# Kernel tuning notes

Hardware: AMD Instinct MI355X
Metric: run time of the kernel (lower is better)

Reference implementation:

```python
import jax, jax.numpy as jnp
import numpy as np

DIM = 1024
HEADS = 16
HEAD_DIM = DIM // HEADS
HIDDEN = 4 * DIM
EPS = 1e-6


def _layer_norm(x, scale, bias):
    mu = jnp.mean(x, axis=-1, keepdims=True)
    var = jnp.mean(jnp.square(x - mu), axis=-1, keepdims=True)
    return (x - mu) * jax.lax.rsqrt(var + EPS) * scale + bias


def setup_inputs() -> dict:
    key = jax.random.key(0)
    ks = jax.random.split(key, 8)
    s = 0.02
    return {
        "x": jax.random.normal(ks[0], (8, 1024, DIM), dtype=jnp.float32),
        "w_qkv": jax.random.normal(ks[1], (DIM, 3 * DIM), dtype=jnp.float32) * s,
        "b_qkv": jnp.zeros((3 * DIM,), jnp.float32),
        "w_proj": jax.random.normal(ks[2], (DIM, DIM), dtype=jnp.float32) * s,
        "b_proj": jnp.zeros((DIM,), jnp.float32),
        "ln1_scale": jnp.ones((DIM,), jnp.float32),
        "ln1_bias": jnp.zeros((DIM,), jnp.float32),
        "ln2_scale": jnp.ones((DIM,), jnp.float32),
        "ln2_bias": jnp.zeros((DIM,), jnp.float32),
        "w_fc1": jax.random.normal(ks[3], (DIM, HIDDEN), dtype=jnp.float32) * s,
        "b_fc1": jnp.zeros((HIDDEN,), jnp.float32),
        "w_fc2": jax.random.normal(ks[4], (HIDDEN, DIM), dtype=jnp.float32) * s,
        "b_fc2": jnp.zeros((DIM,), jnp.float32),
    }


def reference(x, w_qkv, b_qkv, w_proj, b_proj, ln1_scale, ln1_bias,
              ln2_scale, ln2_bias, w_fc1, b_fc1, w_fc2, b_fc2):
    B, N, C = x.shape
    scale = HEAD_DIM ** -0.5

    # --- attention branch ---
    h = _layer_norm(x, ln1_scale, ln1_bias)
    qkv = h @ w_qkv + b_qkv                          # [B,N,3C]
    qkv = qkv.reshape(B, N, 3, HEADS, HEAD_DIM)
    qkv = jnp.transpose(qkv, (2, 0, 3, 1, 4))        # [3,B,H,N,D]
    q, k, v = qkv[0], qkv[1], qkv[2]
    attn = jnp.einsum("bhnd,bhmd->bhnm", q, k) * scale
    attn = jax.nn.softmax(attn, axis=-1)
    o = jnp.einsum("bhnm,bhmd->bhnd", attn, v)       # [B,H,N,D]
    o = jnp.transpose(o, (0, 2, 1, 3)).reshape(B, N, C)
    x = x + (o @ w_proj + b_proj)

    # --- mlp branch ---
    h = _layer_norm(x, ln2_scale, ln2_bias)
    h = jax.nn.gelu(h @ w_fc1 + b_fc1)               # tanh approx, matches flax default
    x = x + (h @ w_fc2 + b_fc2)
    return x
```

## Files before the change

kernel.cpp:

```cpp
#include <hip/hip_runtime.h>

typedef __attribute__((ext_vector_type(8))) short short8;
typedef __attribute__((ext_vector_type(4))) float f32x4;
typedef unsigned short ushort;
typedef unsigned int uint;

#define DIM 1024
#define NSEQ 1024
#define BATCH 8
#define HEADS 16
#define HD 64
#define HIDDEN 4096
#define NROWS (BATCH * NSEQ)

__device__ inline ushort f2bf(float f) {
  uint u = __float_as_uint(f);
  u += 0x7fff + ((u >> 16) & 1);
  return (ushort)(u >> 16);
}

__device__ inline f32x4 zero4() {
  f32x4 z; z[0] = 0.f; z[1] = 0.f; z[2] = 0.f; z[3] = 0.f; return z;
}

__device__ inline float gelu_fast(float x) {
  float u2 = 1.5957691216057308f * (x + 0.044715f * x * x * x);
  float e = __builtin_amdgcn_exp2f(-1.4426950408889634f * u2);
  return x / (1.0f + e);
}

#define GLDS16(g, l)                                                  \
  __builtin_amdgcn_global_load_lds(                                   \
      (const __attribute__((address_space(1))) void*)(g),             \
      (__attribute__((address_space(3))) void*)(l), 16, 0, 0)

__global__ __launch_bounds__(256) void ln_kernel(
    const float* __restrict__ x, const float* __restrict__ sc,
    const float* __restrict__ bi, ushort* __restrict__ out) {
  int row = blockIdx.x;
  int t = threadIdx.x;
  const float4 v = reinterpret_cast<const float4*>(x + (size_t)row * DIM)[t];
  float s = v.x + v.y + v.z + v.w;
  float s2 = v.x * v.x + v.y * v.y + v.z * v.z + v.w * v.w;
#pragma unroll
  for (int off = 32; off >= 1; off >>= 1) {
    s += __shfl_xor(s, off);
    s2 += __shfl_xor(s2, off);
  }
  __shared__ float ps[4], ps2[4];
  int w = t >> 6;
  if ((t & 63) == 0) { ps[w] = s; ps2[w] = s2; }
  __syncthreads();
  s = ps[0] + ps[1] + ps[2] + ps[3];
  s2 = ps2[0] + ps2[1] + ps2[2] + ps2[3];
  float mu = s * (1.0f / DIM);
  float var = s2 * (1.0f / DIM) - mu * mu;
  float rstd = rsqrtf(var + 1e-6f);
  float4 scv = reinterpret_cast<const float4*>(sc)[t];
  float4 biv = reinterpret_cast<const float4*>(bi)[t];
  ushort4 o;
  o.x = f2bf((v.x - mu) * rstd * scv.x + biv.x);
  o.y = f2bf((v.y - mu) * rstd * scv.y + biv.y);
  o.z = f2bf((v.z - mu) * rstd * scv.z + biv.z);
  o.w = f2bf((v.w - mu) * rstd * scv.w + biv.w);
  reinterpret_cast<ushort4*>(out + (size_t)row * DIM)[t] = o;
}

__global__ __launch_bounds__(256) void wtrans_kernel(
    const float* __restrict__ w, ushort* __restrict__ wt, int K, int N) {
  __shared__ float tile[32][33];
  int n0 = blockIdx.x * 32, k0 = blockIdx.y * 32;
  int tx = threadIdx.x & 31, ty = threadIdx.x >> 5;
#pragma unroll
  for (int j = 0; j < 4; j++)
    tile[ty + 8 * j][tx] = w[(size_t)(k0 + ty + 8 * j) * N + n0 + tx];
  __syncthreads();
#pragma unroll
  for (int j = 0; j < 4; j++)
    wt[(size_t)(n0 + ty + 8 * j) * K + k0 + tx] = f2bf(tile[tx][ty + 8 * j]);
}

__global__ __launch_bounds__(256) void vtrans_kernel(
    const ushort* __restrict__ qkv, ushort* __restrict__ vT) {
  __shared__ ushort Ts[64 * 64];
  int bh = blockIdx.y;
  int b = bh >> 4, h = bh & 15;
  int n0 = blockIdx.x * 64;
  int t = threadIdx.x;
  const ushort* src = qkv + (size_t)b * NSEQ * 3072 + 2048 + h * 64;
#pragma unroll
  for (int i = 0; i < 2; i++) {
    int ci = i * 256 + t;
    int rr = ci >> 3, c = ci & 7;
    short8 v = *reinterpret_cast<const short8*>(src + (size_t)(n0 + rr) * 3072 + c * 8);
    *reinterpret_cast<short8*>(&Ts[rr * 64 + ((c ^ (rr >> 3)) & 7) * 8]) = v;
  }
  __syncthreads();
  ushort* dst = vT + (size_t)bh * 64 * NSEQ;
#pragma unroll
  for (int i = 0; i < 2; i++) {
    int ci = i * 256 + t;
    int dd = ci >> 3, c = ci & 7;
    short8 v;
#pragma unroll
    for (int j = 0; j < 8; j++) {
      int nn = c * 8 + j;
      v[j] = (short)Ts[nn * 64 + (((dd >> 3) ^ (nn >> 3)) & 7) * 8 + (dd & 7)];
    }
    *reinterpret_cast<short8*>(dst + (size_t)dd * NSEQ + n0 + c * 8) = v;
  }
}

template <int BN, int EPI>
__global__ __launch_bounds__(512, 2) void gemm256_kernel(
    const ushort* __restrict__ A, const ushort* __restrict__ Bt,
    const float* __restrict__ bias, const float* __restrict__ res,
    void* __restrict__ outp, int M, int N, int K) {
  constexpr int BM = 256, BK = 32;
  constexpr int WM = (BN == 256) ? 2 : 4;
  constexpr int WN = 8 / WM;
  constexpr int MR = (BM / WM) / 16;
  constexpr int NR = (BN / WN) / 16;
  constexpr int AR = 2;
  constexpr int BR = BN / 128;

  __shared__ ushort As[2][BM * BK];
  __shared__ ushort Bs[2][BN * BK];

  int t = threadIdx.x, lane = t & 63, w = t >> 6;
  int wr = w / WN, wc = w % WN;
  int r = lane & 15, g = lane >> 4;
  int m0 = blockIdx.y * BM, n0 = blockIdx.x * BN;
  const ushort* Ab = A + (size_t)m0 * K;
  const ushort* Bb = Bt + (size_t)n0 * K;

  int srow = t >> 2;
  int sgc8 = ((t & 3) ^ (srow & 3)) * 8;
  int swb = (w << 4) * BK;

  f32x4 acc[MR][NR];
#pragma unroll
  for (int mi = 0; mi < MR; mi++)
#pragma unroll
    for (int ni = 0; ni < NR; ni++) acc[mi][ni] = zero4();

  int nkt = K / BK;
#pragma unroll
  for (int p = 0; p < AR; p++)
    GLDS16(Ab + (size_t)(p * 128 + srow) * K + sgc8, &As[0][p * 128 * BK + swb]);
#pragma unroll
  for (int p = 0; p < BR; p++)
    GLDS16(Bb + (size_t)(p * 128 + srow) * K + sgc8, &Bs[0][p * 128 * BK + swb]);
  __syncthreads();

  int cur = 0;
  for (int kt = 0; kt < nkt; kt++) {
    if (kt + 1 < nkt) {
      int ko = (kt + 1) * BK;
#pragma unroll
      for (int p = 0; p < AR; p++)
        GLDS16(Ab + (size_t)(p * 128 + srow) * K + ko + sgc8,
               &As[cur ^ 1][p * 128 * BK + swb]);
#pragma unroll
      for (int p = 0; p < BR; p++)
        GLDS16(Bb + (size_t)(p * 128 + srow) * K + ko + sgc8,
               &Bs[cur ^ 1][p * 128 * BK + swb]);
    }
    short8 a[MR], b[NR];
    int sw = (g ^ (r & 3)) * 8;
#pragma unroll
    for (int mi = 0; mi < MR; mi++)
      a[mi] = *reinterpret_cast<const short8*>(
          &As[cur][(wr * (BM / WM) + mi * 16 + r) * BK + sw]);
#pragma unroll
    for (int ni = 0; ni < NR; ni++)
      b[ni] = *reinterpret_cast<const short8*>(
          &Bs[cur][(wc * (BN / WN) + ni * 16 + r) * BK + sw]);
#pragma unroll
    for (int mi = 0; mi < MR; mi++)
#pragma unroll
      for (int ni = 0; ni < NR; ni++)
        acc[mi][ni] = __builtin_amdgcn_mfma_f32_16x16x32_bf16(a[mi], b[ni], acc[mi][ni], 0, 0, 0);
    __syncthreads();
    cur ^= 1;
  }

  int rg = g * 4;
#pragma unroll
  for (int mi = 0; mi < MR; mi++) {
#pragma unroll
    for (int ni = 0; ni < NR; ni++) {
      int row = m0 + wr * (BM / WM) + mi * 16 + rg;
      int col = n0 + wc * (BN / WN) + ni * 16 + r;
      float bv = bias[col];
#pragma unroll
      for (int j = 0; j < 4; j++) {
        float v = acc[mi][ni][j] + bv;
        if (EPI == 1) v = gelu_fast(v);
        if (EPI == 2) {
          reinterpret_cast<float*>(outp)[(size_t)(row + j) * N + col] =
              v + res[(size_t)(row + j) * N + col];
        } else {
          reinterpret_cast<ushort*>(outp)[(size_t)(row + j) * N + col] = f2bf(v);
        }
      }
    }
  }
}

#define SM_SCALE_L2E 0.18033688f
#define SM_BIAS_L2E 11.54156036f
__global__ __launch_bounds__(256) void attn_kernel(
    const ushort* __restrict__ qkv, const ushort* __restrict__ vT,
    ushort* __restrict__ o) {
  __shared__ ushort Kt[64 * 72];
  __shared__ ushort Vt[64 * 72];
  __shared__ ushort Pl[4][16 * 72];
  int q0 = blockIdx.x * 64, h = blockIdx.y, b = blockIdx.z;
  int t = threadIdx.x, lane = t & 63, w = t >> 6;
  int r = lane & 15, g = lane >> 4;
  const ushort* base = qkv + (size_t)b * NSEQ * 3072 + h * 64;
  const ushort* vbase = vT + (size_t)(b * HEADS + h) * 64 * NSEQ;

  short8 qf[2];
  {
    const ushort* qrow = base + (size_t)(q0 + w * 16 + r) * 3072;
    qf[0] = *reinterpret_cast<const short8*>(qrow + g * 8);
    qf[1] = *reinterpret_cast<const short8*>(qrow + 32 + g * 8);
  }

  float l[4] = {0.f, 0.f, 0.f, 0.f};
  f32x4 oacc[4];
#pragma unroll
  for (int db = 0; db < 4; db++) oacc[db] = zero4();

  int srw = t >> 3, sc8 = (t & 7) * 8;
  for (int kt = 0; kt < NSEQ / 64; kt++) {
    int k0 = kt * 64;
    short8 kreg[2], vreg[2];
#pragma unroll
    for (int i = 0; i < 2; i++) {
      int rw = srw + i * 32;
      kreg[i] = *reinterpret_cast<const short8*>(base + 1024 + (size_t)(k0 + rw) * 3072 + sc8);
      vreg[i] = *reinterpret_cast<const short8*>(vbase + (size_t)rw * NSEQ + k0 + sc8);
    }
    __syncthreads();
#pragma unroll
    for (int i = 0; i < 2; i++) {
      int rw = srw + i * 32;
      *reinterpret_cast<short8*>(&Kt[rw * 72 + sc8]) = kreg[i];
      *reinterpret_cast<short8*>(&Vt[rw * 72 + sc8]) = vreg[i];
    }
    __syncthreads();

#pragma unroll
    for (int kb = 0; kb < 4; kb++) {
      short8 kf0 = *reinterpret_cast<const short8*>(&Kt[(kb * 16 + r) * 72 + g * 8]);
      short8 kf1 = *reinterpret_cast<const short8*>(&Kt[(kb * 16 + r) * 72 + 32 + g * 8]);
      f32x4 z = zero4();
      z = __builtin_amdgcn_mfma_f32_16x16x32_bf16(qf[0], kf0, z, 0, 0, 0);
      z = __builtin_amdgcn_mfma_f32_16x16x32_bf16(qf[1], kf1, z, 0, 0, 0);
#pragma unroll
      for (int j = 0; j < 4; j++) {
        float p = __builtin_amdgcn_exp2f(fmaf(z[j], SM_SCALE_L2E, -SM_BIAS_L2E));
        l[j] += p;
        Pl[w][(g * 4 + j) * 72 + kb * 16 + r] = (ushort)(__float_as_uint(p) >> 16);
      }
    }

#pragma unroll
    for (int ks = 0; ks < 2; ks++) {
      short8 pa = *reinterpret_cast<const short8*>(&Pl[w][r * 72 + ks * 32 + g * 8]);
#pragma unroll
      for (int db = 0; db < 4; db++) {
        short8 vb = *reinterpret_cast<const short8*>(&Vt[(db * 16 + r) * 72 + ks * 32 + g * 8]);
        oacc[db] = __builtin_amdgcn_mfma_f32_16x16x32_bf16(pa, vb, oacc[db], 0, 0, 0);
      }
    }
  }

#pragma unroll
  for (int j = 0; j < 4; j++) {
#pragma unroll
    for (int off = 8; off >= 1; off >>= 1) l[j] += __shfl_xor(l[j], off);
    l[j] = 1.0f / l[j];
  }

#pragma unroll
  for (int db = 0; db < 4; db++)
#pragma unroll
    for (int j = 0; j < 4; j++) {
      size_t row = (size_t)b * NSEQ + q0 + w * 16 + g * 4 + j;
      int col = h * 64 + db * 16 + r;
      o[row * DIM + col] = f2bf(oacc[db][j] * l[j]);
    }
}

extern "C" void kernel_launch(void* const* d_in, const int* in_sizes, int n_in,
                              void* d_out, int out_size, void* d_ws, size_t ws_size,
                              hipStream_t stream) {
  const float* x      = (const float*)d_in[0];
  const float* w_qkv  = (const float*)d_in[1];
  const float* b_qkv  = (const float*)d_in[2];
  const float* w_proj = (const float*)d_in[3];
  const float* b_proj = (const float*)d_in[4];
  const float* ln1s   = (const float*)d_in[5];
  const float* ln1b   = (const float*)d_in[6];
  const float* ln2s   = (const float*)d_in[7];
  const float* ln2b   = (const float*)d_in[8];
  const float* w_fc1  = (const float*)d_in[9];
  const float* b_fc1  = (const float*)d_in[10];
  const float* w_fc2  = (const float*)d_in[11];
  const float* b_fc2  = (const float*)d_in[12];
  float* out = (float*)d_out;

  char* ws = (char*)d_ws;
  ushort* wqkv_t  = (ushort*)(ws);
  ushort* wproj_t = (ushort*)(ws + 6291456);
  ushort* wfc1_t  = (ushort*)(ws + 8388608);
  ushort* wfc2_t  = (ushort*)(ws + 16777216);
  ushort* hbuf    = (ushort*)(ws + 25165824);
  float*  x1      = (float*)(ws + 41943040);
  ushort* vTb     = (ushort*)(ws + 41943040);
  ushort* qkv     = (ushort*)(ws + 75497472);
  ushort* obuf    = (ushort*)(ws + 125829120);
  ushort* fc1a    = qkv;

  wtrans_kernel<<<dim3(3072 / 32, 1024 / 32), 256, 0, stream>>>(w_qkv, wqkv_t, 1024, 3072);
  wtrans_kernel<<<dim3(1024 / 32, 1024 / 32), 256, 0, stream>>>(w_proj, wproj_t, 1024, 1024);
  wtrans_kernel<<<dim3(4096 / 32, 1024 / 32), 256, 0, stream>>>(w_fc1, wfc1_t, 1024, 4096);
  wtrans_kernel<<<dim3(1024 / 32, 4096 / 32), 256, 0, stream>>>(w_fc2, wfc2_t, 4096, 1024);

  ln_kernel<<<NROWS, 256, 0, stream>>>(x, ln1s, ln1b, hbuf);
  gemm256_kernel<128, 0><<<dim3(3072 / 128, NROWS / 256), 512, 0, stream>>>(
      hbuf, wqkv_t, b_qkv, nullptr, qkv, NROWS, 3072, 1024);
  vtrans_kernel<<<dim3(NSEQ / 64, BATCH * HEADS), 256, 0, stream>>>(qkv, vTb);
  attn_kernel<<<dim3(NSEQ / 64, HEADS, BATCH), 256, 0, stream>>>(qkv, vTb, obuf);
  gemm256_kernel<128, 2><<<dim3(1024 / 128, NROWS / 256), 512, 0, stream>>>(
      obuf, wproj_t, b_proj, x, x1, NROWS, 1024, 1024);

  ln_kernel<<<NROWS, 256, 0, stream>>>(x1, ln2s, ln2b, hbuf);
  gemm256_kernel<256, 1><<<dim3(4096 / 256, NROWS / 256), 512, 0, stream>>>(
      hbuf, wfc1_t, b_fc1, nullptr, fc1a, NROWS, 4096, 1024);
  gemm256_kernel<128, 2><<<dim3(1024 / 128, NROWS / 256), 512, 0, stream>>>(
      fc1a, wfc2_t, b_fc2, x1, out, NROWS, 1024, 4096);
}
```

Baseline: 460.6 us.

## Deepen GEMM pipeline to four LDS stages with phased MFMA and tile swizzle

Replaces the double-buffered GEMM main loop with a 4-slot LDS ring that keeps three k-tiles in flight, using explicit vmcnt waits and split phases that interleave global-to-LDS loads with MFMA bursts under raised wave priority. It also remaps workgroup IDs so consecutive blocks share operand tiles in cache, and changes the LDS XOR swizzle to cut bank conflicts. The aim is to hide global load latency and improve L2 reuse. The cost is doubled LDS use, which may lower occupancy, and the hand-counted waitcnt values are fragile.

```diff
diff --git a/kernel.cpp b/kernel.cpp
--- a/kernel.cpp
+++ b/kernel.cpp
@@ -33,6 +33,8 @@
   __builtin_amdgcn_global_load_lds(                                   \
       (const __attribute__((address_space(1))) void*)(g),             \
       (__attribute__((address_space(3))) void*)(l), 16, 0, 0)
+
+#define WAITVM(n) asm volatile("s_waitcnt vmcnt(" #n ")" ::: "memory")
 
 __global__ __launch_bounds__(256) void ln_kernel(
     const float* __restrict__ x, const float* __restrict__ sc,
@@ -121,22 +123,48 @@
   constexpr int WN = 8 / WM;
   constexpr int MR = (BM / WM) / 16;
   constexpr int NR = (BN / WN) / 16;
+  constexpr int PH = MR / 4;
   constexpr int AR = 2;
   constexpr int BR = BN / 128;
-
-  __shared__ ushort As[2][BM * BK];
-  __shared__ ushort Bs[2][BN * BK];
+  static_assert(BN == 256 || BN == 128, "");
+
+  __shared__ ushort As[4][BM * BK];
+  __shared__ ushort Bs[4][BN * BK];
 
   int t = threadIdx.x, lane = t & 63, w = t >> 6;
   int wr = w / WN, wc = w % WN;
   int r = lane & 15, g = lane >> 4;
-  int m0 = blockIdx.y * BM, n0 = blockIdx.x * BN;
+
+  int nwg = gridDim.x * gridDim.y;
+  int flat = blockIdx.y * gridDim.x + blockIdx.x;
+  int swzf = (flat & 7) * (nwg >> 3) + (flat >> 3);
+  int bx = swzf % gridDim.x, by = swzf / gridDim.x;
+  int m0 = by * BM, n0 = bx * BN;
+
   const ushort* Ab = A + (size_t)m0 * K;
   const ushort* Bb = Bt + (size_t)n0 * K;
 
   int srow = t >> 2;
-  int sgc8 = ((t & 3) ^ (srow & 3)) * 8;
+  int sgc8 = (((t & 3) ^ (srow & 3) ^ ((srow >> 2) & 3)) & 3) * 8;
   int swb = (w << 4) * BK;
+  int sw = ((g ^ (r & 3) ^ ((r >> 2) & 3)) & 3) * 8;
+
+  auto stageA = [&](int kt2) {
+    ushort* as = &As[kt2 & 3][0];
+    int ko = kt2 * BK;
+#pragma unroll
+    for (int p = 0; p < AR; p++)
+      GLDS16(Ab + (size_t)(p * 128 + srow) * K + ko + sgc8,
+             as + p * 128 * BK + swb);
+  };
+  auto stageB = [&](int kt2) {
+    ushort* bs = &Bs[kt2 & 3][0];
+    int ko = kt2 * BK;
+#pragma unroll
+    for (int p = 0; p < BR; p++)
+      GLDS16(Bb + (size_t)(p * 128 + srow) * K + ko + sgc8,
+             bs + p * 128 * BK + swb);
+  };
 
   f32x4 acc[MR][NR];
 #pragma unroll
@@ -145,44 +173,61 @@
     for (int ni = 0; ni < NR; ni++) acc[mi][ni] = zero4();
 
   int nkt = K / BK;
-#pragma unroll
-  for (int p = 0; p < AR; p++)
-    GLDS16(Ab + (size_t)(p * 128 + srow) * K + sgc8, &As[0][p * 128 * BK + swb]);
-#pragma unroll
-  for (int p = 0; p < BR; p++)
-    GLDS16(Bb + (size_t)(p * 128 + srow) * K + sgc8, &Bs[0][p * 128 * BK + swb]);
-  __syncthreads();
-
-  int cur = 0;
+
+  stageA(0); stageB(0);
+  stageA(1); stageB(1);
+  stageA(2); stageB(2);
+  if constexpr (BN == 256) WAITVM(8); else WAITVM(6);
+  __builtin_amdgcn_s_barrier();
+  asm volatile("" ::: "memory");
+
   for (int kt = 0; kt < nkt; kt++) {
-    if (kt + 1 < nkt) {
-      int ko = (kt + 1) * BK;
-#pragma unroll
-      for (int p = 0; p < AR; p++)
-        GLDS16(Ab + (size_t)(p * 128 + srow) * K + ko + sgc8,
-               &As[cur ^ 1][p * 128 * BK + swb]);
-#pragma unroll
-      for (int p = 0; p < BR; p++)
-        GLDS16(Bb + (size_t)(p * 128 + srow) * K + ko + sgc8,
-               &Bs[cur ^ 1][p * 128 * BK + swb]);
-    }
-    short8 a[MR], b[NR];
-    int sw = (g ^ (r & 3)) * 8;
-#pragma unroll
-    for (int mi = 0; mi < MR; mi++)
-      a[mi] = *reinterpret_cast<const short8*>(
-          &As[cur][(wr * (BM / WM) + mi * 16 + r) * BK + sw]);
-#pragma unroll
-    for (int ni = 0; ni < NR; ni++)
-      b[ni] = *reinterpret_cast<const short8*>(
-          &Bs[cur][(wc * (BN / WN) + ni * 16 + r) * BK + sw]);
-#pragma unroll
-    for (int mi = 0; mi < MR; mi++)
-#pragma unroll
-      for (int ni = 0; ni < NR; ni++)
-        acc[mi][ni] = __builtin_amdgcn_mfma_f32_16x16x32_bf16(a[mi], b[ni], acc[mi][ni], 0, 0, 0);
-    __syncthreads();
-    cur ^= 1;
+    const ushort* as = &As[kt & 3][0];
+    const ushort* bs = &Bs[kt & 3][0];
+    short8 b[NR];
+#pragma unroll
+    for (int ph = 0; ph < PH; ph++) {
+      if (ph == 0) {
+#pragma unroll
+        for (int ni = 0; ni < NR; ni++)
+          b[ni] = *reinterpret_cast<const short8*>(
+              &bs[(wc * (BN / WN) + ni * 16 + r) * BK + sw]);
+      }
+      short8 a[4];
+#pragma unroll
+      for (int i = 0; i < 4; i++)
+        a[i] = *reinterpret_cast<const short8*>(
+            &as[(wr * (BM / WM) + (ph * 4 + i) * 16 + r) * BK + sw]);
+      if (kt + 3 < nkt) {
+        if constexpr (PH == 2) {
+          if (ph == 0) stageA(kt + 3); else stageB(kt + 3);
+        } else {
+          stageA(kt + 3); stageB(kt + 3);
+        }
+      }
+      if (ph == PH - 1) {
+        if (kt + 3 < nkt) {
+          if constexpr (BN == 256) WAITVM(8); else WAITVM(6);
+        } else if (kt + 2 < nkt) {
+          if constexpr (BN == 256) WAITVM(4); else WAITVM(3);
+        } else if (kt + 1 < nkt) {
+          WAITVM(0);
+        }
+      }
+      __builtin_amdgcn_s_barrier();
+      asm volatile("s_waitcnt lgkmcnt(0)" ::: "memory");
+      __builtin_amdgcn_sched_barrier(0);
+      __builtin_amdgcn_s_setprio(1);
+#pragma unroll
+      for (int i = 0; i < 4; i++)
+#pragma unroll
+        for (int ni = 0; ni < NR; ni++)
+          acc[ph * 4 + i][ni] = __builtin_amdgcn_mfma_f32_16x16x32_bf16(
+              a[i], b[ni], acc[ph * 4 + i][ni], 0, 0, 0);
+      __builtin_amdgcn_s_setprio(0);
+      __builtin_amdgcn_s_barrier();
+      asm volatile("" ::: "memory");
+    }
   }
 
   int rg = g * 4;
```

After: 398.8 us. -13.4%, faster.

## Switch GEMMs to 128x128 tiles with workgroup swizzle and stronger LDS swizzle

Applied to the files above, without the earlier changes.

Replaces the 256-row GEMM tiles (512 threads) with a 128x128 tile kernel of 256 threads and four waves. Each wave computes a 64x64 sub-tile. Block indices are remapped with an XCD-style swizzle so neighbouring blocks land on the same L2, and the LDS XOR pattern now also mixes in row bits to cut bank conflicts. Smaller tiles give more blocks and better occupancy, at the cost of lower arithmetic intensity and more global/L2 traffic per FLOP.

```diff
diff --git a/kernel.cpp b/kernel.cpp
--- a/kernel.cpp
+++ b/kernel.cpp
@@ -111,46 +111,46 @@
   }
 }
 
-template <int BN, int EPI>
-__global__ __launch_bounds__(512, 2) void gemm256_kernel(
+template <int EPI>
+__global__ __launch_bounds__(256, 3) void gemm128_kernel(
     const ushort* __restrict__ A, const ushort* __restrict__ Bt,
     const float* __restrict__ bias, const float* __restrict__ res,
     void* __restrict__ outp, int M, int N, int K) {
-  constexpr int BM = 256, BK = 32;
-  constexpr int WM = (BN == 256) ? 2 : 4;
-  constexpr int WN = 8 / WM;
-  constexpr int MR = (BM / WM) / 16;
-  constexpr int NR = (BN / WN) / 16;
-  constexpr int AR = 2;
-  constexpr int BR = BN / 128;
+  constexpr int BM = 128, BN = 128, BK = 32;
 
   __shared__ ushort As[2][BM * BK];
   __shared__ ushort Bs[2][BN * BK];
 
   int t = threadIdx.x, lane = t & 63, w = t >> 6;
-  int wr = w / WN, wc = w % WN;
+  int wr = w >> 1, wc = w & 1;
   int r = lane & 15, g = lane >> 4;
-  int m0 = blockIdx.y * BM, n0 = blockIdx.x * BN;
+
+  int nwg = gridDim.x * gridDim.y;
+  int flat = blockIdx.y * gridDim.x + blockIdx.x;
+  int swzf = (flat & 7) * (nwg >> 3) + (flat >> 3);
+  int bx = swzf % gridDim.x, by = swzf / gridDim.x;
+  int m0 = by * BM, n0 = bx * BN;
+
   const ushort* Ab = A + (size_t)m0 * K;
   const ushort* Bb = Bt + (size_t)n0 * K;
 
   int srow = t >> 2;
-  int sgc8 = ((t & 3) ^ (srow & 3)) * 8;
-  int swb = (w << 4) * BK;
-
-  f32x4 acc[MR][NR];
-#pragma unroll
-  for (int mi = 0; mi < MR; mi++)
-#pragma unroll
-    for (int ni = 0; ni < NR; ni++) acc[mi][ni] = zero4();
+  int sgc8 = (((t & 3) ^ (srow & 3) ^ ((srow >> 2) & 3)) & 3) * 8;
+  int swb = (t >> 6) * 16 * BK;
+  int sw = ((g ^ (r & 3) ^ ((r >> 2) & 3)) & 3) * 8;
+
+  f32x4 acc[4][4];
+#pragma unroll
+  for (int mi = 0; mi < 4; mi++)
+#pragma unroll
+    for (int ni = 0; ni < 4; ni++) acc[mi][ni] = zero4();
 
   int nkt = K / BK;
 #pragma unroll
-  for (int p = 0; p < AR; p++)
-    GLDS16(Ab + (size_t)(p * 128 + srow) * K + sgc8, &As[0][p * 128 * BK + swb]);
-#pragma unroll
-  for (int p = 0; p < BR; p++)
-    GLDS16(Bb + (size_t)(p * 128 + srow) * K + sgc8, &Bs[0][p * 128 * BK + swb]);
+  for (int p = 0; p < 2; p++) {
+    GLDS16(Ab + (size_t)(p * 64 + srow) * K + sgc8, &As[0][(p * 64) * BK + swb]);
+    GLDS16(Bb + (size_t)(p * 64 + srow) * K + sgc8, &Bs[0][(p * 64) * BK + swb]);
+  }
   __syncthreads();
 
   int cur = 0;
@@ -158,40 +158,39 @@
     if (kt + 1 < nkt) {
       int ko = (kt + 1) * BK;
 #pragma unroll
-      for (int p = 0; p < AR; p++)
-        GLDS16(Ab + (size_t)(p * 128 + srow) * K + ko + sgc8,
-               &As[cur ^ 1][p * 128 * BK + swb]);
-#pragma unroll
-      for (int p = 0; p < BR; p++)
-        GLDS16(Bb + (size_t)(p * 128 + srow) * K + ko + sgc8,
-               &Bs[cur ^ 1][p * 128 * BK + swb]);
-    }
-    short8 a[MR], b[NR];
-    int sw = (g ^ (r & 3)) * 8;
-#pragma unroll
-    for (int mi = 0; mi < MR; mi++)
+      for (int p = 0; p < 2; p++) {
+        GLDS16(Ab + (size_t)(p * 64 + srow) * K + ko + sgc8,
+               &As[cur ^ 1][(p * 64) * BK + swb]);
+        GLDS16(Bb + (size_t)(p * 64 + srow) * K + ko + sgc8,
+               &Bs[cur ^ 1][(p * 64) * BK + swb]);
+      }
+    }
+    short8 a[4], b[4];
+#pragma unroll
+    for (int mi = 0; mi < 4; mi++)
       a[mi] = *reinterpret_cast<const short8*>(
-          &As[cur][(wr * (BM / WM) + mi * 16 + r) * BK + sw]);
-#pragma unroll
-    for (int ni = 0; ni < NR; ni++)
+          &As[cur][(wr * 64 + mi * 16 + r) * BK + sw]);
+#pragma unroll
+    for (int ni = 0; ni < 4; ni++)
       b[ni] = *reinterpret_cast<const short8*>(
-          &Bs[cur][(wc * (BN / WN) + ni * 16 + r) * BK + sw]);
-#pragma unroll
-    for (int mi = 0; mi < MR; mi++)
-#pragma unroll
-      for (int ni = 0; ni < NR; ni++)
-        acc[mi][ni] = __builtin_amdgcn_mfma_f32_16x16x32_bf16(a[mi], b[ni], acc[mi][ni], 0, 0, 0);
+          &Bs[cur][(wc * 64 + ni * 16 + r) * BK + sw]);
+#pragma unroll
+    for (int mi = 0; mi < 4; mi++)
+#pragma unroll
+      for (int ni = 0; ni < 4; ni++)
+        acc[mi][ni] = __builtin_amdgcn_mfma_f32_16x16x32_bf16(
+            a[mi], b[ni], acc[mi][ni], 0, 0, 0);
     __syncthreads();
     cur ^= 1;
   }
 
   int rg = g * 4;
 #pragma unroll
-  for (int mi = 0; mi < MR; mi++) {
-#pragma unroll
-    for (int ni = 0; ni < NR; ni++) {
-      int row = m0 + wr * (BM / WM) + mi * 16 + rg;
-      int col = n0 + wc * (BN / WN) + ni * 16 + r;
+  for (int mi = 0; mi < 4; mi++) {
+#pragma unroll
+    for (int ni = 0; ni < 4; ni++) {
+      int row = m0 + wr * 64 + mi * 16 + rg;
+      int col = n0 + wc * 64 + ni * 16 + r;
       float bv = bias[col];
 #pragma unroll
       for (int j = 0; j < 4; j++) {
@@ -332,16 +331,16 @@
   wtrans_kernel<<<dim3(1024 / 32, 4096 / 32), 256, 0, stream>>>(w_fc2, wfc2_t, 4096, 1024);
 
   ln_kernel<<<NROWS, 256, 0, stream>>>(x, ln1s, ln1b, hbuf);
-  gemm256_kernel<128, 0><<<dim3(3072 / 128, NROWS / 256), 512, 0, stream>>>(
+  gemm128_kernel<0><<<dim3(3072 / 128, NROWS / 128), 256, 0, stream>>>(
       hbuf, wqkv_t, b_qkv, nullptr, qkv, NROWS, 3072, 1024);
   vtrans_kernel<<<dim3(NSEQ / 64, BATCH * HEADS), 256, 0, stream>>>(qkv, vTb);
   attn_kernel<<<dim3(NSEQ / 64, HEADS, BATCH), 256, 0, stream>>>(qkv, vTb, obuf);
-  gemm256_kernel<128, 2><<<dim3(1024 / 128, NROWS / 256), 512, 0, stream>>>(
+  gemm128_kernel<2><<<dim3(1024 / 128, NROWS / 128), 256, 0, stream>>>(
       obuf, wproj_t, b_proj, x, x1, NROWS, 1024, 1024);
 
   ln_kernel<<<NROWS, 256, 0, stream>>>(x1, ln2s, ln2b, hbuf);
-  gemm256_kernel<256, 1><<<dim3(4096 / 256, NROWS / 256), 512, 0, stream>>>(
+  gemm128_kernel<1><<<dim3(4096 / 128, NROWS / 128), 256, 0, stream>>>(
       hbuf, wfc1_t, b_fc1, nullptr, fc1a, NROWS, 4096, 1024);
-  gemm256_kernel<128, 2><<<dim3(1024 / 128, NROWS / 256), 512, 0, stream>>>(
+  gemm128_kernel<2><<<dim3(1024 / 128, NROWS / 128), 256, 0, stream>>>(
       fc1a, wfc2_t, b_fc2, x1, out, NROWS, 1024, 4096);
 }
```

Measured after the change: 414.4 us. -10.0%, faster.
